# Performance work log

Measured on AMD Instinct MI355X. Metric: run time of the kernel, lower is better.

The kernel has to match this reference:

```python
import jax, jax.numpy as jnp
import numpy as np

N = 10000   # num_nodes
E = 320000  # num_edges (avg degree 32)
IN, HID, OUT = 512, 512, 256


def setup_inputs() -> dict:
    key = jax.random.key(0)
    ks = jax.random.split(key, 19)
    rn = lambda k, shape: (jax.random.normal(k, shape, jnp.float32) * 0.05)
    edge_index = jax.random.randint(ks[0], (2, E), 0, N, dtype=jnp.int32)
    return {
        "edge_index": edge_index,
        "w_pe": rn(ks[1], (IN, N)), "b_pe": rn(ks[2], (IN,)),
        "w_self0": rn(ks[3], (HID, IN)), "w_neigh0": rn(ks[4], (HID, IN)), "b0": rn(ks[5], (HID,)),
        "w_res0": rn(ks[6], (HID, IN)), "rb0": rn(ks[7], (HID,)),
        "w_self1": rn(ks[8], (HID, HID)), "w_neigh1": rn(ks[9], (HID, HID)), "b1": rn(ks[10], (HID,)),
        "w_res1": rn(ks[11], (HID, HID)), "rb1": rn(ks[12], (HID,)),
        "w_self2": rn(ks[13], (OUT, HID)), "w_neigh2": rn(ks[14], (OUT, HID)), "b2": rn(ks[15], (OUT,)),
        "w_res2": rn(ks[16], (OUT, HID)), "rb2": rn(ks[17], (OUT,)),
    }


def reference(edge_index, w_pe, b_pe,
              w_self0, w_neigh0, b0, w_res0, rb0,
              w_self1, w_neigh1, b1, w_res1, rb1,
              w_self2, w_neigh2, b2, w_res2, rb2):
    src, dst = edge_index[0], edge_index[1]

    def mean_agg(h):
        # mean of neighbor features per destination node (sparse SAGE aggregation)
        s = jax.ops.segment_sum(h[src], dst, num_segments=N)           # [N, D]
        deg = jax.ops.segment_sum(jnp.ones((E,), h.dtype), dst, num_segments=N)
        return s / jnp.maximum(deg, 1.0)[:, None]

    # pe = Linear(eye(N)) as in the original module
    pe = jnp.eye(N, dtype=w_pe.dtype) @ w_pe.T + b_pe                   # [N, IN]

    layers = [
        (w_self0, w_neigh0, b0, w_res0, rb0),
        (w_self1, w_neigh1, b1, w_res1, rb1),
        (w_self2, w_neigh2, b2, w_res2, rb2),
    ]

    h = pe
    mids = []
    for i, (ws, wn, b, wr, rb) in enumerate(layers):
        h_prev = h
        # SAGEConv (mean): fc_self(h) + fc_neigh(mean_neigh(h))
        h = h @ ws.T + mean_agg(h_prev) @ wn.T + b
        if i != len(layers) - 1:
            h = jax.nn.leaky_relu(h, 0.01)
            # F.dropout with training=False is identity (inference reference)
        h = h + (h_prev @ wr.T + rb)  # residual linear
        mids.append(h)
    return (h, *mids)
```

## Files before the change

kernel.cpp:

```cpp
#include <hip/hip_runtime.h>

#define N_NODES 10000
#define N_EDGES 320000
#define DIN 512
#define DHID 512
#define DOUT 256

typedef __bf16 bf16x8 __attribute__((ext_vector_type(8)));
typedef float f32x4 __attribute__((ext_vector_type(4)));
typedef unsigned short ushort_t;
typedef unsigned int uint_t;

__device__ __forceinline__ float b2f(ushort_t u){
    union { uint_t i; float f; } v; v.i = (uint_t)u << 16; return v.f;
}
__device__ __forceinline__ float blo(uint_t v){
    union { uint_t i; float f; } u; u.i = v << 16; return u.f;
}
__device__ __forceinline__ float bhi(uint_t v){
    union { uint_t i; float f; } u; u.i = v & 0xffff0000u; return u.f;
}
__device__ __forceinline__ ushort_t f2b(float f){
    union { float f; uint_t i; } v; v.f = f;
    uint_t i = v.i;
    return (ushort_t)((i + 0x7fffu + ((i >> 16) & 1u)) >> 16);
}

__device__ __forceinline__ void gll16(const ushort_t* g, ushort_t* l){
    __builtin_amdgcn_global_load_lds(
        (const __attribute__((address_space(1))) unsigned int*)g,
        (__attribute__((address_space(3))) unsigned int*)l,
        16, 0, 0);
}


__global__ void k_zero(int* __restrict__ deg, uint_t* __restrict__ zp){
    int i = blockIdx.x * 256 + threadIdx.x;
    if (i < N_NODES) deg[i] = 0;
    if (i < 256) zp[i] = 0u;
}

__global__ void k_degree(const int* __restrict__ dst, int* __restrict__ deg){
    int e = blockIdx.x * 256 + threadIdx.x;
    if (e < N_EDGES) atomicAdd(&deg[dst[e]], 1);
}

__global__ void k_scan(const int* __restrict__ deg, int* __restrict__ row_ptr,
                       int* __restrict__ cursor){
    __shared__ int part[256];
    int t = threadIdx.x;
    int base = t * 40;
    int loc[40];
    int s = 0;
    #pragma unroll
    for (int i = 0; i < 40; ++i){
        int idx = base + i;
        int v = (idx < N_NODES) ? deg[idx] : 0;
        s += v; loc[i] = s;
    }
    part[t] = s;
    __syncthreads();
    int val = s;
    for (int off = 1; off < 256; off <<= 1){
        int x = (t >= off) ? part[t - off] : 0;
        __syncthreads();
        val += x; part[t] = val;
        __syncthreads();
    }
    int exc = val - s;
    if (t == 0) row_ptr[0] = 0;
    int run = exc;
    #pragma unroll
    for (int i = 0; i < 40; ++i){
        int idx = base + i;
        if (idx < N_NODES){
            row_ptr[idx + 1] = exc + loc[i];
            cursor[idx] = run;
        }
        run = exc + loc[i];
    }
}

__global__ void k_scatter(const int* __restrict__ src, const int* __restrict__ dst,
                          int* __restrict__ cursor, int* __restrict__ srcs){
    int e = blockIdx.x * 256 + threadIdx.x;
    if (e < N_EDGES){
        int p = atomicAdd(&cursor[dst[e]], 1);
        srcs[p] = src[e];
    }
}


struct CvtArgs { const float* s[9]; ushort_t* d[9]; int n[9]; };

__global__ void k_cvt(CvtArgs a){
    int m = blockIdx.y;
    int i = (blockIdx.x * 256 + threadIdx.x) * 8;
    if (i < a.n[m]){
        const float* sp = a.s[m] + i;
        float4 f0 = *(const float4*)sp;
        float4 f1 = *(const float4*)(sp + 4);
        uint4 u;
        u.x = (uint_t)f2b(f0.x) | ((uint_t)f2b(f0.y) << 16);
        u.y = (uint_t)f2b(f0.z) | ((uint_t)f2b(f0.w) << 16);
        u.z = (uint_t)f2b(f1.x) | ((uint_t)f2b(f1.y) << 16);
        u.w = (uint_t)f2b(f1.z) | ((uint_t)f2b(f1.w) << 16);
        *(uint4*)&a.d[m][i] = u;
    }
}


__global__ void k_pe(const float* __restrict__ w_pe, const float* __restrict__ b_pe,
                     ushort_t* __restrict__ h0){
    __shared__ float lt[64][68];
    int t = threadIdx.x;
    int n0 = blockIdx.x * 64, i0 = blockIdx.y * 64;
    int nc = (t & 15) * 4, ir = t >> 4;
    #pragma unroll
    for (int p = 0; p < 4; ++p){
        int i_loc = ir + p * 16;
        float4 v = {0.f, 0.f, 0.f, 0.f};
        if (n0 + nc < N_NODES)
            v = *(const float4*)&w_pe[(size_t)(i0 + i_loc) * N_NODES + n0 + nc];
        lt[nc + 0][i_loc] = v.x;
        lt[nc + 1][i_loc] = v.y;
        lt[nc + 2][i_loc] = v.z;
        lt[nc + 3][i_loc] = v.w;
    }
    __syncthreads();
    int ic = t & 7, nr = t >> 3;
    #pragma unroll
    for (int p = 0; p < 2; ++p){
        int n_loc = nr + p * 32;
        int n = n0 + n_loc;
        if (n < N_NODES){
            uint4 u;
            uint_t w01 = (uint_t)f2b(lt[n_loc][ic*8+0] + b_pe[i0+ic*8+0])
                       | ((uint_t)f2b(lt[n_loc][ic*8+1] + b_pe[i0+ic*8+1]) << 16);
            uint_t w23 = (uint_t)f2b(lt[n_loc][ic*8+2] + b_pe[i0+ic*8+2])
                       | ((uint_t)f2b(lt[n_loc][ic*8+3] + b_pe[i0+ic*8+3]) << 16);
            uint_t w45 = (uint_t)f2b(lt[n_loc][ic*8+4] + b_pe[i0+ic*8+4])
                       | ((uint_t)f2b(lt[n_loc][ic*8+5] + b_pe[i0+ic*8+5]) << 16);
            uint_t w67 = (uint_t)f2b(lt[n_loc][ic*8+6] + b_pe[i0+ic*8+6])
                       | ((uint_t)f2b(lt[n_loc][ic*8+7] + b_pe[i0+ic*8+7]) << 16);
            u.x = w01; u.y = w23; u.z = w45; u.w = w67;
            *(uint4*)&h0[(size_t)n * DIN + i0 + ic * 8] = u;
        }
    }
}


#define AGG_EDGE(e, CH) { \
    int s_ = __builtin_amdgcn_readlane(sr, (e)); \
    uint_t v_ = *(const uint_t*)&X[((size_t)(uint_t)s_ << 9) + col]; \
    CH##0 += blo(v_); CH##1 += bhi(v_); }

__global__ __launch_bounds__(256) void k_agg(
    const ushort_t* __restrict__ X, const int* __restrict__ row_ptr,
    const int* __restrict__ srcs, ushort_t* __restrict__ out, int dummy)
{
    int w = threadIdx.x >> 6, lane = threadIdx.x & 63;
    int n = blockIdx.x * 4 + w;
    int col = blockIdx.y * 128 + lane * 2;
    int beg = row_ptr[n], end = row_ptr[n + 1];
    int deg = end - beg;
    float a0=0.f,a1=0.f, p0=0.f,p1=0.f, c0=0.f,c1=0.f, d0=0.f,d1=0.f;

    for (int base = beg; base < end; base += 64){
        int rem = end - base;
        int sr = (lane < rem) ? srcs[base + lane] : dummy;
        int cnt = rem < 64 ? rem : 64;
        #pragma unroll
        for (int k = 0; k < 4; ++k){
            if (k * 16 < cnt){
                int L = k * 16;
                AGG_EDGE(L + 0,  a) AGG_EDGE(L + 1,  p) AGG_EDGE(L + 2,  c) AGG_EDGE(L + 3,  d)
                AGG_EDGE(L + 4,  a) AGG_EDGE(L + 5,  p) AGG_EDGE(L + 6,  c) AGG_EDGE(L + 7,  d)
                AGG_EDGE(L + 8,  a) AGG_EDGE(L + 9,  p) AGG_EDGE(L + 10, c) AGG_EDGE(L + 11, d)
                AGG_EDGE(L + 12, a) AGG_EDGE(L + 13, p) AGG_EDGE(L + 14, c) AGG_EDGE(L + 15, d)
            }
        }
    }

    float r0 = (a0 + p0) + (c0 + d0);
    float r1 = (a1 + p1) + (c1 + d1);
    float inv = (deg > 0) ? 1.f / (float)deg : 1.f;
    uint_t o = (uint_t)f2b(r0 * inv) | ((uint_t)f2b(r1 * inv) << 16);
    *(uint_t*)&out[(size_t)n * 512 + col] = o;
}


template<int DO, int BN, bool ACT, bool DUAL2, bool WRITE_BF>
__global__ __launch_bounds__(256, 2) void k_layer(
    const ushort_t* __restrict__ X, const ushort_t* __restrict__ G,
    const ushort_t* __restrict__ Ws, const ushort_t* __restrict__ Wn,
    const ushort_t* __restrict__ Wr,
    const float* __restrict__ b, const float* __restrict__ rb,
    float* __restrict__ Y, float* __restrict__ Y2, ushort_t* __restrict__ YB)
{
    constexpr int BM   = 160;
    constexpr int NT   = DO / BN;
    constexpr int WTN  = BN / 32;
    constexpr int NCH  = (2 * BM + 3 * BN) / 16;
    constexpr int CHPW = (NCH + 3) / 4;
    constexpr int OG   = BM * 32;
    constexpr int OS   = 2 * BM * 32;
    constexpr int WS32 = BN * 32;
    constexpr int BUFSZ = OS + 3 * WS32;
    __shared__ __align__(16) ushort_t smem[2][BUFSZ];

    int t = threadIdx.x;
    int bid = blockIdx.x;
    int r8 = bid & 7, q8 = bid >> 3;
    int m_t = (q8 / NT) * 8 + r8;
    int n_t = q8 % NT;
    if (m_t * BM >= N_NODES) return;
    int m0 = m_t * BM, n0 = n_t * BN;

    int lane = t & 63, w = t >> 6;
    int wr = w >> 1, wc = w & 1;

    const ushort_t* gptr[CHPW];
    int coff[CHPW];
    bool gv[CHPW];
    int rl = lane >> 2, sl = (lane & 3) * 8;
    #pragma unroll
    for (int i = 0; i < CHPW; ++i){
        int qq = w * CHPW + i;
        gv[i] = (qq < NCH);
        int qc = gv[i] ? qq : 0;
        const ushort_t* gA; int rowbase, off;
        if (qc < 10)      { gA = X;  rowbase = m0 + qc * 16;        off = qc * 512; }
        else if (qc < 20) { gA = G;  rowbase = m0 + (qc - 10) * 16; off = OG + (qc - 10) * 512; }
        else {
            int q2 = qc - 20;
            int sec = q2 / (BN / 16), wi = q2 % (BN / 16);
            gA = (sec == 0) ? Ws : (sec == 1) ? Wn : Wr;
            rowbase = n0 + wi * 16;
            off = OS + sec * WS32 + wi * 512;
        }
        gptr[i] = gA + (size_t)(rowbase + rl) * 512 + sl;
        coff[i] = off;
    }

    f32x4 accS[5][WTN] = {}, accG[5][WTN] = {}, accR[5][WTN] = {};
    int r16 = lane & 15;
    int arow = wr * 80 + r16;
    int brow = wc * (BN / 2) + r16;
    int kk = (lane >> 4) * 8;

    #pragma unroll
    for (int i = 0; i < CHPW; ++i) if (gv[i]) gll16(gptr[i], &smem[0][coff[i]]);
    __syncthreads();

    int cur = 0;
    for (int ks = 0; ks < 16; ++ks){
        if (ks < 15){
            int k0 = (ks + 1) * 32;
            #pragma unroll
            for (int i = 0; i < CHPW; ++i) if (gv[i]) gll16(gptr[i] + k0, &smem[cur ^ 1][coff[i]]);
        }

        const ushort_t* sb = smem[cur];
        bf16x8 ax[5], ag[5], bs[WTN], bn_[WTN], brr[WTN];
        #pragma unroll
        for (int m = 0; m < 5; ++m){
            ax[m] = *(const bf16x8*)&sb[(arow + m * 16) * 32 + kk];
            ag[m] = *(const bf16x8*)&sb[OG + (arow + m * 16) * 32 + kk];
        }
        #pragma unroll
        for (int n = 0; n < WTN; ++n){
            bs[n]  = *(const bf16x8*)&sb[OS            + (brow + n * 16) * 32 + kk];
            bn_[n] = *(const bf16x8*)&sb[OS + WS32     + (brow + n * 16) * 32 + kk];
            brr[n] = *(const bf16x8*)&sb[OS + 2 * WS32 + (brow + n * 16) * 32 + kk];
        }
        #pragma unroll
        for (int m = 0; m < 5; ++m)
            #pragma unroll
            for (int n = 0; n < WTN; ++n){
                accS[m][n] = __builtin_amdgcn_mfma_f32_16x16x32_bf16(ax[m], bs[n],  accS[m][n], 0, 0, 0);
                accG[m][n] = __builtin_amdgcn_mfma_f32_16x16x32_bf16(ag[m], bn_[n], accG[m][n], 0, 0, 0);
                accR[m][n] = __builtin_amdgcn_mfma_f32_16x16x32_bf16(ax[m], brr[n], accR[m][n], 0, 0, 0);
            }

        __syncthreads();
        cur ^= 1;
    }

    int col_l = lane & 15;
    int row_l = (lane >> 4) * 4;
    #pragma unroll
    for (int n = 0; n < WTN; ++n){
        int col = n0 + wc * (BN / 2) + n * 16 + col_l;
        float bb = b[col], rbb = rb[col];
        #pragma unroll
        for (int m = 0; m < 5; ++m){
            #pragma unroll
            for (int j = 0; j < 4; ++j){
                int row = m0 + wr * 80 + m * 16 + row_l + j;
                if (row < N_NODES){
                    float v = accS[m][n][j] + accG[m][n][j] + bb;
                    if (ACT) v = (v > 0.f) ? v : 0.01f * v;
                    v += accR[m][n][j] + rbb;
                    Y[(size_t)row * DO + col] = v;
                    if (DUAL2) Y2[(size_t)row * DO + col] = v;
                    if (WRITE_BF) YB[(size_t)row * DO + col] = f2b(v);
                }
            }
        }
    }
}


extern "C" void kernel_launch(void* const* d_in, const int* in_sizes, int n_in,
                              void* d_out, int out_size, void* d_ws, size_t ws_size,
                              hipStream_t stream) {
    const int* edge  = (const int*)d_in[0];
    const int* e_src = edge;
    const int* e_dst = edge + N_EDGES;
    const float* w_pe = (const float*)d_in[1];
    const float* b_pe = (const float*)d_in[2];
    const float* ws0 = (const float*)d_in[3];
    const float* wn0 = (const float*)d_in[4];
    const float* b0  = (const float*)d_in[5];
    const float* wr0 = (const float*)d_in[6];
    const float* rb0 = (const float*)d_in[7];
    const float* ws1 = (const float*)d_in[8];
    const float* wn1 = (const float*)d_in[9];
    const float* b1  = (const float*)d_in[10];
    const float* wr1 = (const float*)d_in[11];
    const float* rb1 = (const float*)d_in[12];
    const float* ws2 = (const float*)d_in[13];
    const float* wn2 = (const float*)d_in[14];
    const float* b2  = (const float*)d_in[15];
    const float* wr2 = (const float*)d_in[16];
    const float* rb2 = (const float*)d_in[17];

    char* wsb = (char*)d_ws;
    ushort_t* h0   = (ushort_t*)wsb;
    ushort_t* hb   = (ushort_t*)(wsb + 10240000);
    ushort_t* aggb = (ushort_t*)(wsb + 20480000);
    ushort_t* wbf  = (ushort_t*)(wsb + 30720000);
    int* deg     = (int*)(wsb + 34652160);
    int* row_ptr = deg + 10016;
    int* cursor  = row_ptr + 10016;
    int* srcs    = cursor + 10016;
    uint_t* zp   = (uint_t*)(wsb + 36052992);
    const int dummy_h0 = 35208;
    const int dummy_hb = 25208;

    ushort_t* wbf0s = wbf;
    ushort_t* wbf0n = wbf + 262144;
    ushort_t* wbf0r = wbf + 524288;
    ushort_t* wbf1s = wbf + 786432;
    ushort_t* wbf1n = wbf + 1048576;
    ushort_t* wbf1r = wbf + 1310720;
    ushort_t* wbf2s = wbf + 1572864;
    ushort_t* wbf2n = wbf + 1703936;
    ushort_t* wbf2r = wbf + 1835008;

    float* out  = (float*)d_out;
    float* fin  = out;
    float* mid0 = out + 2560000;
    float* mid1 = out + 7680000;
    float* mid2 = out + 12800000;

    k_zero   <<<40, 256, 0, stream>>>(deg, zp);
    k_degree <<<1250, 256, 0, stream>>>(e_dst, deg);
    k_scan   <<<1, 256, 0, stream>>>(deg, row_ptr, cursor);
    k_scatter<<<1250, 256, 0, stream>>>(e_src, e_dst, cursor, srcs);

    CvtArgs ca;
    ca.s[0]=ws0; ca.s[1]=wn0; ca.s[2]=wr0;
    ca.s[3]=ws1; ca.s[4]=wn1; ca.s[5]=wr1;
    ca.s[6]=ws2; ca.s[7]=wn2; ca.s[8]=wr2;
    ca.d[0]=wbf0s; ca.d[1]=wbf0n; ca.d[2]=wbf0r;
    ca.d[3]=wbf1s; ca.d[4]=wbf1n; ca.d[5]=wbf1r;
    ca.d[6]=wbf2s; ca.d[7]=wbf2n; ca.d[8]=wbf2r;
    for (int i = 0; i < 6; ++i) ca.n[i] = 262144;
    for (int i = 6; i < 9; ++i) ca.n[i] = 131072;
    k_cvt<<<dim3(128, 9), 256, 0, stream>>>(ca);

    k_pe<<<dim3(157, 8), 256, 0, stream>>>(w_pe, b_pe, h0);

    k_agg<<<dim3(2500, 4), 256, 0, stream>>>(h0, row_ptr, srcs, aggb, dummy_h0);
    k_layer<512, 64, true,  false, true ><<<dim3(512), 256, 0, stream>>>(
        h0, aggb, wbf0s, wbf0n, wbf0r, b0, rb0, mid0, nullptr, hb);

    k_agg<<<dim3(2500, 4), 256, 0, stream>>>(hb, row_ptr, srcs, aggb, dummy_hb);
    k_layer<512, 64, true,  false, true ><<<dim3(512), 256, 0, stream>>>(
        hb, aggb, wbf1s, wbf1n, wbf1r, b1, rb1, mid1, nullptr, h0);

    k_agg<<<dim3(2500, 4), 256, 0, stream>>>(h0, row_ptr, srcs, aggb, dummy_h0);
    k_layer<256, 32, false, true,  false><<<dim3(512), 256, 0, stream>>>(
        h0, aggb, wbf2s, wbf2n, wbf2r, b2, rb2, mid2, fin, nullptr);
}
```

Measured before the change: 228.8 us.

## Reorder last layer: project before aggregating and merge self and residual weights

For the final layer, which has no activation, the self and residual weights are summed into one matrix during bf16 conversion. The neighbour projection is applied before aggregation, so the gather runs over 256-wide bf16 projected features instead of 512-wide inputs. A new GEMM kernel computes both the projected features and the self-plus-residual term. A fused aggregation kernel then adds the mean of neighbour projections and writes both outputs. This halves gather traffic and removes one GEMM from the last layer, but it changes rounding because the projections are stored in bf16 before averaging.

```diff
diff --git a/kernel.cpp b/kernel.cpp
--- a/kernel.cpp
+++ b/kernel.cpp
@@ -91,7 +91,7 @@
 }
 
 
-struct CvtArgs { const float* s[9]; ushort_t* d[9]; int n[9]; };
+struct CvtArgs { const float* s[8]; const float* s2[8]; ushort_t* d[8]; int n[8]; };
 
 __global__ void k_cvt(CvtArgs a){
     int m = blockIdx.y;
@@ -100,6 +100,13 @@
         const float* sp = a.s[m] + i;
         float4 f0 = *(const float4*)sp;
         float4 f1 = *(const float4*)(sp + 4);
+        if (a.s2[m]){
+            const float* sq = a.s2[m] + i;
+            float4 g0 = *(const float4*)sq;
+            float4 g1 = *(const float4*)(sq + 4);
+            f0.x += g0.x; f0.y += g0.y; f0.z += g0.z; f0.w += g0.w;
+            f1.x += g1.x; f1.y += g1.y; f1.z += g1.z; f1.w += g1.w;
+        }
         uint4 u;
         u.x = (uint_t)f2b(f0.x) | ((uint_t)f2b(f0.y) << 16);
         u.y = (uint_t)f2b(f0.z) | ((uint_t)f2b(f0.w) << 16);
@@ -190,13 +197,58 @@
 }
 
 
-template<int DO, int BN, bool ACT, bool DUAL2, bool WRITE_BF>
+#define AGGF_EDGE(e, CH) { \
+    int s_ = __builtin_amdgcn_readlane(sr, (e)); \
+    uint_t v_ = *(const uint_t*)&P[((size_t)(uint_t)s_ << 8) + col]; \
+    CH##0 += blo(v_); CH##1 += bhi(v_); }
+
+__global__ __launch_bounds__(256) void k_aggf(
+    const ushort_t* __restrict__ P, const int* __restrict__ row_ptr,
+    const int* __restrict__ srcs, const float* __restrict__ Q,
+    float* __restrict__ fin, float* __restrict__ mid2, int dummy)
+{
+    int w = threadIdx.x >> 6, lane = threadIdx.x & 63;
+    int n = blockIdx.x * 4 + w;
+    int col = blockIdx.y * 128 + lane * 2;
+    int beg = row_ptr[n], end = row_ptr[n + 1];
+    int deg = end - beg;
+    float a0=0.f,a1=0.f, p0=0.f,p1=0.f, c0=0.f,c1=0.f, d0=0.f,d1=0.f;
+
+    for (int base = beg; base < end; base += 64){
+        int rem = end - base;
+        int sr = (lane < rem) ? srcs[base + lane] : dummy;
+        int cnt = rem < 64 ? rem : 64;
+        #pragma unroll
+        for (int k = 0; k < 4; ++k){
+            if (k * 16 < cnt){
+                int L = k * 16;
+                AGGF_EDGE(L + 0,  a) AGGF_EDGE(L + 1,  p) AGGF_EDGE(L + 2,  c) AGGF_EDGE(L + 3,  d)
+                AGGF_EDGE(L + 4,  a) AGGF_EDGE(L + 5,  p) AGGF_EDGE(L + 6,  c) AGGF_EDGE(L + 7,  d)
+                AGGF_EDGE(L + 8,  a) AGGF_EDGE(L + 9,  p) AGGF_EDGE(L + 10, c) AGGF_EDGE(L + 11, d)
+                AGGF_EDGE(L + 12, a) AGGF_EDGE(L + 13, p) AGGF_EDGE(L + 14, c) AGGF_EDGE(L + 15, d)
+            }
+        }
+    }
+
+    float r0 = (a0 + p0) + (c0 + d0);
+    float r1 = (a1 + p1) + (c1 + d1);
+    float inv = (deg > 0) ? 1.f / (float)deg : 1.f;
+    float2 q = *(const float2*)&Q[(size_t)n * 256 + col];
+    float2 o;
+    o.x = q.x + r0 * inv;
+    o.y = q.y + r1 * inv;
+    *(float2*)&fin [(size_t)n * 256 + col] = o;
+    *(float2*)&mid2[(size_t)n * 256 + col] = o;
+}
+
+
+template<int DO, int BN, bool ACT, bool WRITE_BF>
 __global__ __launch_bounds__(256, 2) void k_layer(
     const ushort_t* __restrict__ X, const ushort_t* __restrict__ G,
     const ushort_t* __restrict__ Ws, const ushort_t* __restrict__ Wn,
     const ushort_t* __restrict__ Wr,
     const float* __restrict__ b, const float* __restrict__ rb,
-    float* __restrict__ Y, float* __restrict__ Y2, ushort_t* __restrict__ YB)
+    float* __restrict__ Y, ushort_t* __restrict__ YB)
 {
     constexpr int BM   = 160;
     constexpr int NT   = DO / BN;
@@ -303,9 +355,103 @@
                     if (ACT) v = (v > 0.f) ? v : 0.01f * v;
                     v += accR[m][n][j] + rbb;
                     Y[(size_t)row * DO + col] = v;
-                    if (DUAL2) Y2[(size_t)row * DO + col] = v;
                     if (WRITE_BF) YB[(size_t)row * DO + col] = f2b(v);
                 }
+            }
+        }
+    }
+}
+
+
+__global__ __launch_bounds__(256, 2) void k_layer2(
+    const ushort_t* __restrict__ X,
+    const ushort_t* __restrict__ Wn, const ushort_t* __restrict__ Wsr,
+    const float* __restrict__ b, const float* __restrict__ rb,
+    ushort_t* __restrict__ Pout, float* __restrict__ Qout)
+{
+    constexpr int BM = 160, BN = 32, NT = DOUT / BN;
+    constexpr int NCH = 10 + 2 * (BN / 16);
+    constexpr int CHPW = 4;
+    constexpr int OWN = BM * 32;
+    constexpr int OWS = OWN + BN * 32;
+    constexpr int BUFSZ = OWS + BN * 32;
+    __shared__ __align__(16) ushort_t smem[2][BUFSZ];
+
+    int t = threadIdx.x;
+    int bid = blockIdx.x;
+    int r8 = bid & 7, q8 = bid >> 3;
+    int m_t = (q8 / NT) * 8 + r8;
+    int n_t = q8 % NT;
+    if (m_t * BM >= N_NODES) return;
+    int m0 = m_t * BM, n0 = n_t * BN;
+
+    int lane = t & 63, w = t >> 6;
+    int wr = w >> 1, wc = w & 1;
+
+    const ushort_t* gptr[CHPW];
+    int coff[CHPW];
+    bool gv[CHPW];
+    int rl = lane >> 2, sl = (lane & 3) * 8;
+    #pragma unroll
+    for (int i = 0; i < CHPW; ++i){
+        int qq = w * CHPW + i;
+        gv[i] = (qq < NCH);
+        int qc = gv[i] ? qq : 0;
+        const ushort_t* gA; int rowbase, off;
+        if (qc < 10)      { gA = X;   rowbase = m0 + qc * 16;        off = qc * 512; }
+        else if (qc < 12) { gA = Wn;  rowbase = n0 + (qc - 10) * 16; off = OWN + (qc - 10) * 512; }
+        else              { gA = Wsr; rowbase = n0 + (qc - 12) * 16; off = OWS + (qc - 12) * 512; }
+        gptr[i] = gA + (size_t)(rowbase + rl) * 512 + sl;
+        coff[i] = off;
+    }
+
+    f32x4 accP[5] = {}, accQ[5] = {};
+    int r16 = lane & 15;
+    int arow = wr * 80 + r16;
+    int brow = wc * 16 + r16;
+    int kk = (lane >> 4) * 8;
+
+    #pragma unroll
+    for (int i = 0; i < CHPW; ++i) if (gv[i]) gll16(gptr[i], &smem[0][coff[i]]);
+    __syncthreads();
+
+    int cur = 0;
+    for (int ks = 0; ks < 16; ++ks){
+        if (ks < 15){
+            int k0 = (ks + 1) * 32;
+            #pragma unroll
+            for (int i = 0; i < CHPW; ++i) if (gv[i]) gll16(gptr[i] + k0, &smem[cur ^ 1][coff[i]]);
+        }
+
+        const ushort_t* sb = smem[cur];
+        bf16x8 ax[5];
+        #pragma unroll
+        for (int m = 0; m < 5; ++m)
+            ax[m] = *(const bf16x8*)&sb[(arow + m * 16) * 32 + kk];
+        bf16x8 bn_ = *(const bf16x8*)&sb[OWN + brow * 32 + kk];
+        bf16x8 bsr = *(const bf16x8*)&sb[OWS + brow * 32 + kk];
+        #pragma unroll
+        for (int m = 0; m < 5; ++m){
+            accP[m] = __builtin_amdgcn_mfma_f32_16x16x32_bf16(ax[m], bn_, accP[m], 0, 0, 0);
+            accQ[m] = __builtin_amdgcn_mfma_f32_16x16x32_bf16(ax[m], bsr, accQ[m], 0, 0, 0);
+        }
+
+        __syncthreads();
+        cur ^= 1;
+    }
+
+    int col_l = lane & 15;
+    int row_l = (lane >> 4) * 4;
+    int col = n0 + wc * 16 + col_l;
+    float bb = b[col] + rb[col];
+    #pragma unroll
+    for (int m = 0; m < 5; ++m){
+        #pragma unroll
+        for (int j = 0; j < 4; ++j){
+            int row = m0 + wr * 80 + m * 16 + row_l + j;
+            if (row < N_NODES){
+                Qout[(size_t)row * DOUT + col] = accQ[m][j] + bb;
+                Pout[(size_t)row * DOUT + col] = f2b(accP[m][j]);
             }
         }
     }
@@ -348,6 +494,7 @@
     uint_t* zp   = (uint_t*)(wsb + 36052992);
     const int dummy_h0 = 35208;
     const int dummy_hb = 25208;
+    const int dummy_pb = 30416;
 
     ushort_t* wbf0s = wbf;
     ushort_t* wbf0n = wbf + 262144;
@@ -355,15 +502,15 @@
     ushort_t* wbf1s = wbf + 786432;
     ushort_t* wbf1n = wbf + 1048576;
     ushort_t* wbf1r = wbf + 1310720;
-    ushort_t* wbf2s = wbf + 1572864;
-    ushort_t* wbf2n = wbf + 1703936;
-    ushort_t* wbf2r = wbf + 1835008;
+    ushort_t* wbf2n = wbf + 1572864;
+    ushort_t* wbf2sr= wbf + 1703936;
 
     float* out  = (float*)d_out;
     float* fin  = out;
     float* mid0 = out + 2560000;
     float* mid1 = out + 7680000;
     float* mid2 = out + 12800000;
+    ushort_t* pb = aggb;
 
     k_zero   <<<40, 256, 0, stream>>>(deg, zp);
     k_degree <<<1250, 256, 0, stream>>>(e_dst, deg);
@@ -373,25 +520,26 @@
     CvtArgs ca;
     ca.s[0]=ws0; ca.s[1]=wn0; ca.s[2]=wr0;
     ca.s[3]=ws1; ca.s[4]=wn1; ca.s[5]=wr1;
-    ca.s[6]=ws2; ca.s[7]=wn2; ca.s[8]=wr2;
+    ca.s[6]=wn2; ca.s[7]=ws2;
+    for (int i = 0; i < 8; ++i) ca.s2[i] = nullptr;
+    ca.s2[7] = wr2;
     ca.d[0]=wbf0s; ca.d[1]=wbf0n; ca.d[2]=wbf0r;
     ca.d[3]=wbf1s; ca.d[4]=wbf1n; ca.d[5]=wbf1r;
-    ca.d[6]=wbf2s; ca.d[7]=wbf2n; ca.d[8]=wbf2r;
+    ca.d[6]=wbf2n; ca.d[7]=wbf2sr;
     for (int i = 0; i < 6; ++i) ca.n[i] = 262144;
-    for (int i = 6; i < 9; ++i) ca.n[i] = 131072;
-    k_cvt<<<dim3(128, 9), 256, 0, stream>>>(ca);
+    ca.n[6] = 131072; ca.n[7] = 131072;
+    k_cvt<<<dim3(128, 8), 256, 0, stream>>>(ca);
 
     k_pe<<<dim3(157, 8), 256, 0, stream>>>(w_pe, b_pe, h0);
 
     k_agg<<<dim3(2500, 4), 256, 0, stream>>>(h0, row_ptr, srcs, aggb, dummy_h0);
-    k_layer<512, 64, true,  false, true ><<<dim3(512), 256, 0, stream>>>(
-        h0, aggb, wbf0s, wbf0n, wbf0r, b0, rb0, mid0, nullptr, hb);
+    k_layer<512, 64, true, true ><<<dim3(512), 256, 0, stream>>>(
+        h0, aggb, wbf0s, wbf0n, wbf0r, b0, rb0, mid0, hb);
 
     k_agg<<<dim3(2500, 4), 256, 0, stream>>>(hb, row_ptr, srcs, aggb, dummy_hb);
-    k_layer<512, 64, true,  false, true ><<<dim3(512), 256, 0, stream>>>(
-        hb, aggb, wbf1s, wbf1n, wbf1r, b1, rb1, mid1, nullptr, h0);
-
-    k_agg<<<dim3(2500, 4), 256, 0, stream>>>(h0, row_ptr, srcs, aggb, dummy_h0);
-    k_layer<256, 32, false, true,  false><<<dim3(512), 256, 0, stream>>>(
-        h0, aggb, wbf2s, wbf2n, wbf2r, b2, rb2, mid2, fin, nullptr);
-}
+    k_layer<512, 64, true, true ><<<dim3(512), 256, 0, stream>>>(
+        hb, aggb, wbf1s, wbf1n, wbf1r, b1, rb1, mid1, h0);
+
+    k_layer2<<<dim3(512), 256, 0, stream>>>(h0, wbf2n, wbf2sr, b2, rb2, pb, mid2);
+    k_aggf<<<dim3(2500, 2), 256, 0, stream>>>(pb, row_ptr, srcs, mid2, fin, mid2, dummy_pb);
+}
```

After: 214.1 us. 1.07x faster.
